# Optimization experiments

Hardware: AMD Instinct MI355X
Metric: run time of the kernel (lower is better)

The kernel has to match this reference:

```python
import jax, jax.numpy as jnp
import numpy as np

BETA = 0.25


def setup_inputs() -> dict:
    key = jax.random.key(0)
    k1, k2 = jax.random.split(key)
    z = jax.random.normal(k1, (16, 256, 32, 32), dtype=jnp.float32)
    # nn.Embedding init: uniform(-1/K, 1/K) with K = in_channels = 16384
    K, D = 16384, 256
    emb = jax.random.uniform(k2, (K, D), dtype=jnp.float32,
                             minval=-1.0 / K, maxval=1.0 / K)
    return {"z": z, "emb": emb}


def reference(z, emb):
    K, D = emb.shape
    # NCHW -> NHWC, flatten to tokens
    zp = jnp.transpose(z, (0, 2, 3, 1))            # [B,H,W,D]
    zf = zp.reshape(-1, D)                          # [N,D]
    # squared L2 distances: ||z||^2 + ||e||^2 - 2 z.e  -> [N,K]
    d = (jnp.sum(zf * zf, axis=1, keepdims=True)
         + jnp.sum(emb * emb, axis=1)
         - 2.0 * jnp.matmul(zf, emb.T))
    idx = jnp.argmin(d, axis=1)                     # [N] int
    # gather via direct lookup (equivalent to one-hot @ emb)
    z_q = emb[idx].reshape(zp.shape)                # [B,H,W,D]
    # commitment + codebook loss
    loss = (jnp.mean((jax.lax.stop_gradient(z_q) - zp) ** 2)
            + BETA * jnp.mean((z_q - jax.lax.stop_gradient(zp)) ** 2))
    # perplexity from code usage histogram (same as mean of one-hot rows)
    counts = jax.ops.segment_sum(jnp.ones_like(idx, dtype=jnp.float32), idx,
                                 num_segments=K)
    e_mean = counts / idx.shape[0]
    perplexity = jnp.exp(-jnp.sum(e_mean * jnp.log(e_mean + 1e-10)))
    # straight-through estimator, back to NCHW
    z_q_st = zp + jax.lax.stop_gradient(z_q - zp)
    z_q_out = jnp.transpose(z_q_st, (0, 3, 1, 2))   # [B,D,H,W]
    return z_q_out, loss, perplexity, idx
```

## Files before the change

kernel.cpp:

```cpp
#include <hip/hip_runtime.h>
#include <math.h>

#define NTOK   16384
#define DDIM   256
#define HWD    1024
#define CHW    262144
#define MARGIN 3.0e-4f
#define CLIPF  5.5f
#define QS     (127.0f/5.5f)
#define EQS    2080768.0f
#define SCALE  (5.5f/(127.0f*127.0f*16384.0f))

#define WS_TI8   0u
#define WS_CI8   4194304u
#define WS_M1    8388608u
#define WS_M2    16777216u
#define WS_ARG   25165824u
#define WS_FLG   29360128u
#define WS_EE    29376512u
#define WS_ZZ    29442048u
#define WS_IDX   29507584u
#define WS_CNT   29573120u
#define WS_SUM   29638656u

typedef __attribute__((ext_vector_type(4)))  int   i32x4;
typedef __attribute__((ext_vector_type(16))) char  c16;

__global__ __launch_bounds__(256) void k_prep(const float* __restrict__ z,
                                              const float* __restrict__ emb,
                                              char* __restrict__ Ti8,
                                              char* __restrict__ Ci8,
                                              float* __restrict__ zz,
                                              float* __restrict__ ee,
                                              float* __restrict__ zt,
                                              unsigned char* __restrict__ flags) {
  const int bid = blockIdx.x;
  const int tid = threadIdx.x;
  const int t64 = tid & 63, chunk = tid >> 6;
  if (bid < 256) {
    __shared__ double part[4][64];
    __shared__ int   fpart[4][64];
    const int n = bid * 64 + t64;
    const int b = n >> 10, hw = n & 1023;
    const float* zp = z + (size_t)b * CHW + hw;
    float tmp[64];
    double s = 0.0;
    int clip = 0;
    #pragma unroll
    for (int j = 0; j < 64; ++j) {
      const float f = zp[(size_t)(chunk * 64 + j) * HWD];
      tmp[j] = f;
      s += (double)f * (double)f;
      clip |= (fabsf(f) > CLIPF) ? 1 : 0;
    }
    c16 q[4];
    #pragma unroll
    for (int sl = 0; sl < 4; ++sl)
      #pragma unroll
      for (int j = 0; j < 16; ++j)
        q[sl][j] = (char)(int)rintf(fminf(fmaxf(tmp[sl * 16 + j], -CLIPF), CLIPF) * QS);
    const int rl = n & 127, tile = n >> 7;
    char* dst = Ti8 + (size_t)tile * 32768 + chunk * 8192 + rl * 64;
    const int sw = ((rl >> 1) & 3) << 4;
    #pragma unroll
    for (int sl = 0; sl < 4; ++sl) *(c16*)(dst + ((sl * 16) ^ sw)) = q[sl];
    float* ztp = zt + (size_t)n * 256 + chunk * 64;
    #pragma unroll
    for (int j4 = 0; j4 < 16; ++j4) *(float4*)(ztp + j4 * 4) = *(float4*)&tmp[j4 * 4];
    part[chunk][t64] = s;
    fpart[chunk][t64] = clip;
    __syncthreads();
    if (tid < 64) {
      zz[n] = (float)(part[0][t64] + part[1][t64] + part[2][t64] + part[3][t64]);
      flags[n] = (unsigned char)(fpart[0][t64] | fpart[1][t64] | fpart[2][t64] | fpart[3][t64]);
    }
  } else {
    __shared__ float rows[64][257];
    __shared__ double part2[4][64];
    const int k0 = (bid - 256) * 64;
    for (int i = tid; i < 16384; i += 256)
      rows[i >> 8][i & 255] = emb[(size_t)k0 * DDIM + i];
    __syncthreads();
    const int code = k0 + t64;
    double s = 0.0;
    c16 q[4];
    #pragma unroll
    for (int sl = 0; sl < 4; ++sl)
      #pragma unroll
      for (int j = 0; j < 16; ++j) {
        const float f = rows[t64][chunk * 64 + sl * 16 + j];
        q[sl][j] = (char)(int)rintf(f * EQS);
        s += (double)f * (double)f;
      }
    const int rl = code & 127, tile = code >> 7;
    char* dst = Ci8 + (size_t)tile * 32768 + chunk * 8192 + rl * 64;
    const int sw = ((rl >> 1) & 3) << 4;
    #pragma unroll
    for (int sl = 0; sl < 4; ++sl) *(c16*)(dst + ((sl * 16) ^ sw)) = q[sl];
    part2[chunk][t64] = s;
    __syncthreads();
    if (tid < 64)
      ee[code] = (float)(part2[0][t64] + part2[1][t64] + part2[2][t64] + part2[3][t64]);
  }
}

__global__ __launch_bounds__(256) void k_mdist(
    const char* __restrict__ tokimg, const char* __restrict__ codimg,
    _Float16* __restrict__ M1, _Float16* __restrict__ M2,
    unsigned char* __restrict__ ARG) {
  __shared__ __attribute__((aligned(16))) char lds[65536];
  const int raw = blockIdx.x;
  const int p = raw & 7, local = raw >> 3;
  const int ctile = p * 16 + (local & 15);
  const int ttile = local >> 4;
  const int tid = threadIdx.x;
  const int w = tid >> 6, lane = tid & 63;
  const int wr = w >> 1, wc = w & 1;
  const int fr = lane & 15, fq = lane >> 4;
  const char* asrc = codimg + (size_t)ctile * 32768;
  const char* bsrc = tokimg + (size_t)ttile * 32768;

  #pragma unroll
  for (int r = 0; r < 8; ++r) {
    const int u = r * 256 + tid;
    __builtin_amdgcn_global_load_lds(
        (const __attribute__((address_space(1))) void*)(asrc + u * 16),
        (__attribute__((address_space(3))) void*)(lds + u * 16), 16, 0, 0);
  }
  #pragma unroll
  for (int r = 0; r < 8; ++r) {
    const int u = r * 256 + tid;
    __builtin_amdgcn_global_load_lds(
        (const __attribute__((address_space(1))) void*)(bsrc + u * 16),
        (__attribute__((address_space(3))) void*)(lds + 32768 + u * 16), 16, 0, 0);
  }

  int aoff[4][4], boff[4][4];
  #pragma unroll
  for (int m = 0; m < 4; ++m)
    #pragma unroll
    for (int kc = 0; kc < 4; ++kc) {
      const int c = wr * 64 + m * 16 + fr;
      aoff[m][kc] = kc * 8192 + c * 64 + ((fq * 16) ^ (((c >> 1) & 3) << 4));
      const int t = wc * 64 + m * 16 + fr;
      boff[m][kc] = 32768 + kc * 8192 + t * 64 + ((fq * 16) ^ (((t >> 1) & 3) << 4));
    }

  i32x4 acc[4][4];
  #pragma unroll
  for (int m = 0; m < 4; ++m)
    #pragma unroll
    for (int n = 0; n < 4; ++n) acc[m][n] = (i32x4)0;

  __syncthreads();

  #pragma unroll
  for (int kc = 0; kc < 4; ++kc) {
    i32x4 a[4], b[4];
    #pragma unroll
    for (int m = 0; m < 4; ++m) a[m] = *(const i32x4*)(lds + aoff[m][kc]);
    #pragma unroll
    for (int n = 0; n < 4; ++n) b[n] = *(const i32x4*)(lds + boff[n][kc]);
    #pragma unroll
    for (int m = 0; m < 4; ++m)
      #pragma unroll
      for (int n = 0; n < 4; ++n)
        acc[m][n] = __builtin_amdgcn_mfma_i32_16x16x64_i8(a[m], b[n], acc[m][n], 0, 0, 0);
  }

  __syncthreads();
  _Float16* m1l = (_Float16*)lds;
  _Float16* m2l = (_Float16*)(lds + 512);
  unsigned char* agl = (unsigned char*)(lds + 1024);
  #pragma unroll
  for (int n = 0; n < 4; ++n) {
    int v1 = acc[0][n][0], a1 = fq * 4, v2 = (int)0x80000000;
    #pragma unroll
    for (int m = 0; m < 4; ++m)
      #pragma unroll
      for (int j = 0; j < 4; ++j) {
        if (m == 0 && j == 0) continue;
        const int v = acc[m][n][j];
        const int id = m * 16 + fq * 4 + j;
        if (v > v1) { v2 = v1; v1 = v; a1 = id; }
        else if (v > v2) v2 = v;
      }
    #pragma unroll
    for (int off = 16; off <= 32; off <<= 1) {
      const int o1 = __shfl_xor(v1, off, 64);
      const int oa = __shfl_xor(a1, off, 64);
      const int o2 = __shfl_xor(v2, off, 64);
      if (o1 > v1) { v2 = v1 > o2 ? v1 : o2; v1 = o1; a1 = oa; }
      else v2 = v2 > o2 ? v2 : o2;
    }
    if (lane < 16) {
      const int tl = wc * 64 + n * 16 + fr;
      m1l[tl * 2 + wr] = (_Float16)(-2.0f * SCALE * (float)v1);
      m2l[tl * 2 + wr] = (_Float16)(-2.0f * SCALE * (float)v2);
      agl[tl * 2 + wr] = (unsigned char)a1;
    }
  }
  __syncthreads();
  if (tid < 128) {
    const int tok = ttile * 128 + tid;
    *(unsigned int*)((char*)M1 + (size_t)tok * 512 + ctile * 4) =
        *(const unsigned int*)(m1l + tid * 2);
    M2[(size_t)(ctile * 2) * NTOK + tok]     = m2l[tid * 2];
    M2[(size_t)(ctile * 2 + 1) * NTOK + tok] = m2l[tid * 2 + 1];
    ARG[(size_t)(ctile * 2) * NTOK + tok]     = agl[tid * 2];
    ARG[(size_t)(ctile * 2 + 1) * NTOK + tok] = agl[tid * 2 + 1];
  }
}

__global__ __launch_bounds__(256) void k_pick(
    const float* __restrict__ zt, const float* __restrict__ emb,
    const float* __restrict__ zz, const float* __restrict__ ee,
    const _Float16* __restrict__ M1, const _Float16* __restrict__ M2,
    const unsigned char* __restrict__ ARG, const unsigned char* __restrict__ flags,
    int* __restrict__ idx, float* __restrict__ out_idxf) {
  __shared__ float zrow[256];
  __shared__ int clist[2048];
  __shared__ int ccnt;
  __shared__ float wm[4];
  __shared__ unsigned long long bests[16];
  const int tid = threadIdx.x;
  const int w = tid >> 6, lane = tid & 63;
  const int g16 = lane >> 4, l16 = lane & 15;
  const int G = w * 4 + g16;
  for (int ni = 0; ni < 8; ++ni) {
    const int n = blockIdx.x * 8 + ni;
    __syncthreads();
    if (tid == 0) ccnt = 0;
    zrow[tid] = zt[(size_t)n * 256 + tid];
    const float ta = (float)M1[(size_t)n * 256 + tid];
    float mr = ta;
    #pragma unroll
    for (int o = 32; o; o >>= 1) mr = fminf(mr, __shfl_xor(mr, o, 64));
    if (lane == 0) wm[w] = mr;
    __syncthreads();
    const int ex0 = flags[n];
    const float thr = ex0 ? 3.0e38f
                          : fminf(fminf(wm[0], wm[1]), fminf(wm[2], wm[3])) + MARGIN;
    if (!ex0 && ta <= thr) {
      const float m2v = (float)M2[(size_t)tid * NTOK + n];
      if (m2v > thr) {
        const int pos = atomicAdd(&ccnt, 1);
        if (pos < 2048) clist[pos] = tid * 64 + (int)ARG[(size_t)tid * NTOK + n];
      } else {
        const int pos = atomicAdd(&ccnt, 64);
        if (pos + 64 <= 2048)
          for (int i = 0; i < 64; ++i) clist[pos + i] = tid * 64 + i;
      }
    }
    __syncthreads();
    const int doEx = ex0 || (ccnt > 2048);
    const int nc = doEx ? 16384 : ccnt;
    const float zzn = zz[n];
    unsigned long long best = ~0ull;
    for (int ci = 0; ci < nc; ci += 16) {
      int k;
      if (doEx) k = ci + G;
      else { const int sl = ci + G; k = clist[sl < nc ? sl : 0]; }
      const float* er = emb + (size_t)k * DDIM;
      double s = 0.0;
      #pragma unroll
      for (int qq = 0; qq < 4; ++qq) {
        const float4 ev = *(const float4*)(er + qq * 64 + l16 * 4);
        const float4 zv = *(const float4*)(&zrow[qq * 64 + l16 * 4]);
        s += (double)zv.x * (double)ev.x + (double)zv.y * (double)ev.y
           + (double)zv.z * (double)ev.z + (double)zv.w * (double)ev.w;
      }
      #pragma unroll
      for (int o = 8; o; o >>= 1) s += __shfl_xor(s, o, 16);
      if (l16 == 0) {
        const float mm = (float)s;
        const float d = (zzn + ee[k]) - 2.0f * mm;
        const unsigned long long c =
            ((unsigned long long)__float_as_uint(d) << 32) | (unsigned int)k;
        if (c < best) best = c;
      }
    }
    if (l16 == 0) bests[G] = best;
    __syncthreads();
    if (tid == 0) {
      unsigned long long bb = bests[0];
      #pragma unroll
      for (int i = 1; i < 16; ++i) bb = bests[i] < bb ? bests[i] : bb;
      const int k0 = (int)(bb & 0xffffffffu);
      idx[n] = k0;
      out_idxf[n] = (float)k0;
    }
  }
}

__global__ __launch_bounds__(256) void k_scatter(
    const float* __restrict__ z, const float* __restrict__ emb,
    const int* __restrict__ idx, float* __restrict__ out_zq,
    int* __restrict__ counts, double* __restrict__ sums) {
  __shared__ float et[64][257];
  __shared__ int sidx[64];
  __shared__ double w4[4];
  const int tg = blockIdx.x;
  const int n0 = tg * 64;
  const int b = n0 >> 10, hw0 = n0 & 1023;
  const int tid = threadIdx.x;
  if (tid < 64) sidx[tid] = idx[n0 + tid];
  __syncthreads();
  for (int i = tid; i < 16384; i += 256) {
    const int t = i >> 8, d = i & 255;
    et[t][d] = emb[(size_t)sidx[t] * DDIM + d];
  }
  __syncthreads();
  const float* zb = z + (size_t)b * CHW + hw0;
  float* ob = out_zq + (size_t)b * CHW + hw0;
  double s = 0.0;
  for (int i = tid; i < 16384; i += 256) {
    const int d = i >> 6, t = i & 63;
    const float v = et[t][d];
    const float diff = v - zb[(size_t)d * HWD + t];
    ob[(size_t)d * HWD + t] = v;
    s += (double)diff * (double)diff;
  }
  #pragma unroll
  for (int o = 32; o; o >>= 1) s += __shfl_xor(s, o, 64);
  const int wd = tid >> 6, lane = tid & 63;
  if (lane == 0) w4[wd] = s;
  __syncthreads();
  if (tid == 0) atomicAdd(&sums[0], w4[0] + w4[1] + w4[2] + w4[3]);
  if (tid < 64) atomicAdd(&counts[sidx[tid]], 1);
}

__global__ __launch_bounds__(256) void k_hist(const int* __restrict__ counts,
                                              double* __restrict__ sums) {
  const int i = blockIdx.x * 256 + threadIdx.x;
  const float em = (float)counts[i] * (1.0f / 16384.0f);
  const float term = em * logf(em + 1e-10f);
  double s = (double)term;
  #pragma unroll
  for (int o = 32; o; o >>= 1) s += __shfl_xor(s, o, 64);
  __shared__ double w4[4];
  const int wid = threadIdx.x >> 6, lane = threadIdx.x & 63;
  if (lane == 0) w4[wid] = s;
  __syncthreads();
  if (threadIdx.x == 0) atomicAdd(&sums[1], w4[0] + w4[1] + w4[2] + w4[3]);
}

__global__ void k_final(const double* __restrict__ sums,
                        float* __restrict__ out_loss,
                        float* __restrict__ out_perp) {
  if (threadIdx.x == 0) {
    out_loss[0] = (float)(1.25 * sums[0] / 4194304.0);
    out_perp[0] = (float)exp(-sums[1]);
  }
}

extern "C" void kernel_launch(void* const* d_in, const int* in_sizes, int n_in,
                              void* d_out, int out_size, void* d_ws, size_t ws_size,
                              hipStream_t stream) {
  const float* z   = (const float*)d_in[0];
  const float* emb = (const float*)d_in[1];
  float* out      = (float*)d_out;
  float* out_zq   = out;
  float* out_loss = out + 4194304;
  float* out_perp = out + 4194305;
  float* out_idxf = out + 4194306;
  float* zt       = out;

  char* ws = (char*)d_ws;
  char* Ti8 = ws + WS_TI8;
  char* Ci8 = ws + WS_CI8;
  _Float16* M1 = (_Float16*)(ws + WS_M1);
  _Float16* M2 = (_Float16*)(ws + WS_M2);
  unsigned char* ARG = (unsigned char*)(ws + WS_ARG);
  unsigned char* flags = (unsigned char*)(ws + WS_FLG);
  float*  ee      = (float*)(ws + WS_EE);
  float*  zz      = (float*)(ws + WS_ZZ);
  int*    idx     = (int*)  (ws + WS_IDX);
  int*    counts  = (int*)  (ws + WS_CNT);
  double* sums    = (double*)(ws + WS_SUM);

  hipMemsetAsync(counts, 0, 65536 + 16, stream);

  k_prep <<<512, 256, 0, stream>>>(z, emb, Ti8, Ci8, zz, ee, zt, flags);
  k_mdist<<<16384, 256, 0, stream>>>(Ti8, Ci8, M1, M2, ARG);
  k_pick <<<2048, 256, 0, stream>>>(zt, emb, zz, ee, M1, M2, ARG, flags, idx, out_idxf);
  k_scatter<<<256, 256, 0, stream>>>(z, emb, idx, out_zq, counts, sums);
  k_hist <<<64, 256, 0, stream>>>(counts, sums);
  k_final<<<1, 64, 0, stream>>>(sums, out_loss, out_perp);
}
```

Before: 221.9 us.

## Keep codebook fragments in registers and loop k_mdist over double-buffered token tiles

```diff
diff --git a/kernel.cpp b/kernel.cpp
--- a/kernel.cpp
+++ b/kernel.cpp
@@ -25,6 +25,12 @@
 
 typedef __attribute__((ext_vector_type(4)))  int   i32x4;
 typedef __attribute__((ext_vector_type(16))) char  c16;
+
+__device__ __forceinline__ void top2m(int& a1, int& a2, const int b1, const int b2) {
+  const int mn = min(a1, b1);
+  a1 = max(a1, b1);
+  a2 = max(max(a2, b2), mn);
+}
 
 __global__ __launch_bounds__(256) void k_prep(const float* __restrict__ z,
                                               const float* __restrict__ emb,
@@ -92,11 +98,9 @@
         q[sl][j] = (char)(int)rintf(f * EQS);
         s += (double)f * (double)f;
       }
-    const int rl = code & 127, tile = code >> 7;
-    char* dst = Ci8 + (size_t)tile * 32768 + chunk * 8192 + rl * 64;
-    const int sw = ((rl >> 1) & 3) << 4;
-    #pragma unroll
-    for (int sl = 0; sl < 4; ++sl) *(c16*)(dst + ((sl * 16) ^ sw)) = q[sl];
+    char* dst = Ci8 + (size_t)code * 256 + chunk * 64;
+    #pragma unroll
+    for (int sl = 0; sl < 4; ++sl) *(c16*)(dst + sl * 16) = q[sl];
     part2[chunk][t64] = s;
     __syncthreads();
     if (tid < 64)
@@ -105,110 +109,122 @@
 }
 
 __global__ __launch_bounds__(256) void k_mdist(
-    const char* __restrict__ tokimg, const char* __restrict__ codimg,
+    const char* __restrict__ tokimg, const char* __restrict__ codrows,
     _Float16* __restrict__ M1, _Float16* __restrict__ M2,
     unsigned char* __restrict__ ARG) {
-  __shared__ __attribute__((aligned(16))) char lds[65536];
+  __shared__ __attribute__((aligned(16))) char ldsB[65536];
+  __shared__ _Float16 m1l[256];
+  __shared__ _Float16 m2l[256];
+  __shared__ unsigned char agl[256];
   const int raw = blockIdx.x;
-  const int p = raw & 7, local = raw >> 3;
-  const int ctile = p * 16 + (local & 15);
-  const int ttile = local >> 4;
+  const int p = raw & 7;
+  const int ctile = p * 16 + ((raw >> 3) & 15);
+  const int tgrp = raw >> 7;
   const int tid = threadIdx.x;
   const int w = tid >> 6, lane = tid & 63;
   const int wr = w >> 1, wc = w & 1;
   const int fr = lane & 15, fq = lane >> 4;
-  const char* asrc = codimg + (size_t)ctile * 32768;
-  const char* bsrc = tokimg + (size_t)ttile * 32768;
-
+
+  i32x4 afr[4][4];
+  {
+    const char* ab = codrows + (size_t)(ctile * 128 + wr * 64 + fr) * 256 + fq * 16;
+    #pragma unroll
+    for (int m = 0; m < 4; ++m)
+      #pragma unroll
+      for (int kc = 0; kc < 4; ++kc)
+        afr[m][kc] = *(const i32x4*)(ab + m * 16 * 256 + kc * 64);
+  }
+
+  int boff[4][4];
   #pragma unroll
-  for (int r = 0; r < 8; ++r) {
-    const int u = r * 256 + tid;
-    __builtin_amdgcn_global_load_lds(
-        (const __attribute__((address_space(1))) void*)(asrc + u * 16),
-        (__attribute__((address_space(3))) void*)(lds + u * 16), 16, 0, 0);
-  }
-  #pragma unroll
-  for (int r = 0; r < 8; ++r) {
-    const int u = r * 256 + tid;
-    __builtin_amdgcn_global_load_lds(
-        (const __attribute__((address_space(1))) void*)(bsrc + u * 16),
-        (__attribute__((address_space(3))) void*)(lds + 32768 + u * 16), 16, 0, 0);
-  }
-
-  int aoff[4][4], boff[4][4];
-  #pragma unroll
-  for (int m = 0; m < 4; ++m)
+  for (int n = 0; n < 4; ++n)
     #pragma unroll
     for (int kc = 0; kc < 4; ++kc) {
-      const int c = wr * 64 + m * 16 + fr;
-      aoff[m][kc] = kc * 8192 + c * 64 + ((fq * 16) ^ (((c >> 1) & 3) << 4));
-      const int t = wc * 64 + m * 16 + fr;
-      boff[m][kc] = 32768 + kc * 8192 + t * 64 + ((fq * 16) ^ (((t >> 1) & 3) << 4));
-    }
-
-  i32x4 acc[4][4];
-  #pragma unroll
-  for (int m = 0; m < 4; ++m)
-    #pragma unroll
-    for (int n = 0; n < 4; ++n) acc[m][n] = (i32x4)0;
-
+      const int t = wc * 64 + n * 16 + fr;
+      boff[n][kc] = kc * 8192 + t * 64 + ((fq * 16) ^ (((t >> 1) & 3) << 4));
+    }
+
+  #define STAGEB(buf, tt)                                                             \
+    {                                                                                 \
+      const char* src = tokimg + (size_t)(tt) * 32768;                                \
+      char* dstb = ldsB + (buf) * 32768;                                              \
+      _Pragma("unroll")                                                               \
+      for (int r = 0; r < 8; ++r) {                                                   \
+        const int u = r * 256 + tid;                                                  \
+        __builtin_amdgcn_global_load_lds(                                             \
+            (const __attribute__((address_space(1))) void*)(src + u * 16),            \
+            (__attribute__((address_space(3))) void*)(dstb + u * 16), 16, 0, 0);      \
+      }                                                                               \
+    }
+
+  STAGEB(0, tgrp * 8);
   __syncthreads();
 
-  #pragma unroll
-  for (int kc = 0; kc < 4; ++kc) {
-    i32x4 a[4], b[4];
-    #pragma unroll
-    for (int m = 0; m < 4; ++m) a[m] = *(const i32x4*)(lds + aoff[m][kc]);
-    #pragma unroll
-    for (int n = 0; n < 4; ++n) b[n] = *(const i32x4*)(lds + boff[n][kc]);
+  const int fq4 = fq * 4;
+  for (int it = 0; it < 8; ++it) {
+    const int ttile = tgrp * 8 + it;
+    if (it < 7) STAGEB((it + 1) & 1, ttile + 1);
+    const char* bufb = ldsB + (it & 1) * 32768;
+
+    i32x4 acc[4][4];
     #pragma unroll
     for (int m = 0; m < 4; ++m)
       #pragma unroll
-      for (int n = 0; n < 4; ++n)
-        acc[m][n] = __builtin_amdgcn_mfma_i32_16x16x64_i8(a[m], b[n], acc[m][n], 0, 0, 0);
-  }
-
-  __syncthreads();
-  _Float16* m1l = (_Float16*)lds;
-  _Float16* m2l = (_Float16*)(lds + 512);
-  unsigned char* agl = (unsigned char*)(lds + 1024);
-  #pragma unroll
-  for (int n = 0; n < 4; ++n) {
-    int v1 = acc[0][n][0], a1 = fq * 4, v2 = (int)0x80000000;
-    #pragma unroll
-    for (int m = 0; m < 4; ++m)
-      #pragma unroll
-      for (int j = 0; j < 4; ++j) {
-        if (m == 0 && j == 0) continue;
-        const int v = acc[m][n][j];
-        const int id = m * 16 + fq * 4 + j;
-        if (v > v1) { v2 = v1; v1 = v; a1 = id; }
-        else if (v > v2) v2 = v;
-      }
-    #pragma unroll
-    for (int off = 16; off <= 32; off <<= 1) {
-      const int o1 = __shfl_xor(v1, off, 64);
-      const int oa = __shfl_xor(a1, off, 64);
-      const int o2 = __shfl_xor(v2, off, 64);
-      if (o1 > v1) { v2 = v1 > o2 ? v1 : o2; v1 = o1; a1 = oa; }
-      else v2 = v2 > o2 ? v2 : o2;
-    }
-    if (lane < 16) {
-      const int tl = wc * 64 + n * 16 + fr;
-      m1l[tl * 2 + wr] = (_Float16)(-2.0f * SCALE * (float)v1);
-      m2l[tl * 2 + wr] = (_Float16)(-2.0f * SCALE * (float)v2);
-      agl[tl * 2 + wr] = (unsigned char)a1;
-    }
-  }
-  __syncthreads();
-  if (tid < 128) {
-    const int tok = ttile * 128 + tid;
-    *(unsigned int*)((char*)M1 + (size_t)tok * 512 + ctile * 4) =
-        *(const unsigned int*)(m1l + tid * 2);
-    M2[(size_t)(ctile * 2) * NTOK + tok]     = m2l[tid * 2];
-    M2[(size_t)(ctile * 2 + 1) * NTOK + tok] = m2l[tid * 2 + 1];
-    ARG[(size_t)(ctile * 2) * NTOK + tok]     = agl[tid * 2];
-    ARG[(size_t)(ctile * 2 + 1) * NTOK + tok] = agl[tid * 2 + 1];
+      for (int n = 0; n < 4; ++n) acc[m][n] = (i32x4)0;
+
+    #pragma unroll
+    for (int kc = 0; kc < 4; ++kc) {
+      i32x4 b[4];
+      #pragma unroll
+      for (int n = 0; n < 4; ++n) b[n] = *(const i32x4*)(bufb + boff[n][kc]);
+      #pragma unroll
+      for (int m = 0; m < 4; ++m)
+        #pragma unroll
+        for (int n = 0; n < 4; ++n)
+          acc[m][n] = __builtin_amdgcn_mfma_i32_16x16x64_i8(afr[m][kc], b[n], acc[m][n], 0, 0, 0);
+    }
+
+    #pragma unroll
+    for (int n = 0; n < 4; ++n) {
+      int p1[8], p2[8];
+      #pragma unroll
+      for (int m = 0; m < 4; ++m)
+        #pragma unroll
+        for (int jj = 0; jj < 2; ++jj) {
+          const int k0 = (acc[m][n][2 * jj]     << 8) | (m * 16 + fq4 + 2 * jj);
+          const int k1 = (acc[m][n][2 * jj + 1] << 8) | (m * 16 + fq4 + 2 * jj + 1);
+          p1[m * 2 + jj] = max(k0, k1);
+          p2[m * 2 + jj] = min(k0, k1);
+        }
+      top2m(p1[0], p2[0], p1[1], p2[1]); top2m(p1[2], p2[2], p1[3], p2[3]);
+      top2m(p1[4], p2[4], p1[5], p2[5]); top2m(p1[6], p2[6], p1[7], p2[7]);
+      top2m(p1[0], p2[0], p1[2], p2[2]); top2m(p1[4], p2[4], p1[6], p2[6]);
+      top2m(p1[0], p2[0], p1[4], p2[4]);
+      int k1 = p1[0], k2 = p2[0];
+      #pragma unroll
+      for (int off = 16; off <= 32; off <<= 1) {
+        const int o1 = __shfl_xor(k1, off, 64);
+        const int o2 = __shfl_xor(k2, off, 64);
+        top2m(k1, k2, o1, o2);
+      }
+      if (lane < 16) {
+        const int tl = wc * 64 + n * 16 + fr;
+        m1l[tl * 2 + wr] = (_Float16)(-2.0f * SCALE * (float)(k1 >> 8));
+        m2l[tl * 2 + wr] = (_Float16)(-2.0f * SCALE * (float)(k2 >> 8));
+        agl[tl * 2 + wr] = (unsigned char)(k1 & 255);
+      }
+    }
+    __syncthreads();
+    if (tid < 128) {
+      const int tok = ttile * 128 + tid;
+      *(unsigned int*)((char*)M1 + (size_t)tok * 512 + ctile * 4) =
+          *(const unsigned int*)(m1l + tid * 2);
+      M2[(size_t)(ctile * 2) * NTOK + tok]     = m2l[tid * 2];
+      M2[(size_t)(ctile * 2 + 1) * NTOK + tok] = m2l[tid * 2 + 1];
+      ARG[(size_t)(ctile * 2) * NTOK + tok]     = agl[tid * 2];
+      ARG[(size_t)(ctile * 2 + 1) * NTOK + tok] = agl[tid * 2 + 1];
+    }
+    __syncthreads();
   }
 }
 
@@ -382,7 +398,7 @@
   hipMemsetAsync(counts, 0, 65536 + 16, stream);
 
   k_prep <<<512, 256, 0, stream>>>(z, emb, Ti8, Ci8, zz, ee, zt, flags);
-  k_mdist<<<16384, 256, 0, stream>>>(Ti8, Ci8, M1, M2, ARG);
+  k_mdist<<<2048, 256, 0, stream>>>(Ti8, Ci8, M1, M2, ARG);
   k_pick <<<2048, 256, 0, stream>>>(zt, emb, zz, ee, M1, M2, ARG, flags, idx, out_idxf);
   k_scatter<<<256, 256, 0, stream>>>(z, emb, idx, out_zq, counts, sums);
   k_hist <<<64, 256, 0, stream>>>(counts, sums);
```

Measured after the change: 208.7 us. 5.9% less time.
